# Optimization experiments

Measured on AMD Instinct MI355X. Metric: run time of the kernel, lower is better.

The kernel has to match this reference:

```python
import jax, jax.numpy as jnp
import numpy as np

N_NODES = 512
STATE_DIM = 16
MESSAGE_DIM = 32
HID_MSG = 64
HID_RO = 64
N_STEPS = 5


def setup_inputs() -> dict:
    key = jax.random.key(0)
    ks = jax.random.split(key, 16)
    s, m, hm, hr = STATE_DIM, MESSAGE_DIM, HID_MSG, HID_RO
    gru_in = s + m
    k_gru = 1.0 / np.sqrt(s)
    inp = {
        'J': jax.random.normal(ks[0], (N_NODES, N_NODES), jnp.float32),
        'b': jax.random.normal(ks[1], (N_NODES,), jnp.float32),
        # message MLP (torch init: weight ~ N(0, 0.1), bias = 0)
        'W1': 0.1 * jax.random.normal(ks[2], (hm, 2 * s + 3), jnp.float32),
        'b1': jnp.zeros((hm,), jnp.float32),
        'W2': 0.1 * jax.random.normal(ks[3], (hm, hm), jnp.float32),
        'b2': jnp.zeros((hm,), jnp.float32),
        'W3': 0.1 * jax.random.normal(ks[4], (m, hm), jnp.float32),
        'b3': jnp.zeros((m,), jnp.float32),
        # GRUCell params (torch default: U(-1/sqrt(hidden), 1/sqrt(hidden)))
        'W_ih': jax.random.uniform(ks[5], (3 * s, gru_in), jnp.float32, -k_gru, k_gru),
        'b_ih': jnp.zeros((3 * s,), jnp.float32),
        'W_hh': jax.random.uniform(ks[6], (3 * s, s), jnp.float32, -k_gru, k_gru),
        'b_hh': jnp.zeros((3 * s,), jnp.float32),
        # readout MLP
        'Wr1': 0.1 * jax.random.normal(ks[7], (hr, s), jnp.float32),
        'br1': jnp.zeros((hr,), jnp.float32),
        'Wr2': 0.1 * jax.random.normal(ks[8], (hr, hr), jnp.float32),
        'br2': jnp.zeros((hr,), jnp.float32),
        'Wr3': 0.1 * jax.random.normal(ks[9], (2, hr), jnp.float32),
        'br3': jnp.zeros((2,), jnp.float32),
    }
    return inp


def _gru_cell(x, h, W_ih, b_ih, W_hh, b_hh):
    s = h.shape[-1]
    gi = x @ W_ih.T + b_ih  # (n, 3s)
    gh = h @ W_hh.T + b_hh  # (n, 3s)
    ir, iz, in_ = gi[:, :s], gi[:, s:2 * s], gi[:, 2 * s:]
    hr, hz, hn = gh[:, :s], gh[:, s:2 * s], gh[:, 2 * s:]
    r = jax.nn.sigmoid(ir + hr)
    z = jax.nn.sigmoid(iz + hz)
    n = jnp.tanh(in_ + r * hn)
    return (1.0 - z) * n + z * h


def reference(J, b, W1, b1, W2, b2, W3, b3, W_ih, b_ih, W_hh, b_hh,
              Wr1, br1, Wr2, br2, Wr3, br3):
    n = J.shape[0]
    s = W_hh.shape[1]
    # Split first message-MLP layer by input blocks [h_i | h_j | J_ij | b_i | b_j]
    # so we never materialize the (n, n, 2s+3) feature tensor.
    W1_hi = W1[:, :s]            # (hm, s)
    W1_hj = W1[:, s:2 * s]       # (hm, s)
    w_J = W1[:, 2 * s]           # (hm,)
    w_bi = W1[:, 2 * s + 1]      # (hm,)
    w_bj = W1[:, 2 * s + 2]      # (hm,)
    # static per-pair part of layer-1 preactivation: (n, n, hm)
    static1 = (J[:, :, None] * w_J
               + b[:, None, None] * w_bi
               + b[None, :, None] * w_bj
               + b1)

    h0 = jnp.zeros((n, s), jnp.float32)

    def step(h, _):
        pre = (h @ W1_hi.T)[:, None, :] + (h @ W1_hj.T)[None, :, :] + static1
        x = jax.nn.relu(pre)                      # (n, n, hm)
        x = jax.nn.relu(x @ W2.T + b2)            # (n, n, hm)
        msg = x @ W3.T + b3                       # (n, n, m)
        m_j = msg.sum(axis=0)                     # sum over i -> (n, m)
        gru_in = jnp.concatenate([h, m_j], axis=1)
        h_new = _gru_cell(gru_in, h, W_ih, b_ih, W_hh, b_hh)
        return h_new, None

    h, _ = jax.lax.scan(step, h0, None, length=N_STEPS)

    y = jax.nn.relu(h @ Wr1.T + br1)
    y = jax.nn.relu(y @ Wr2.T + br2)
    y = jax.nn.sigmoid(y @ Wr3.T + br3)           # (n, 2)
    y = y / jnp.sum(y, axis=1, keepdims=True)
    return y
```

## Files before the change

### kernel.cpp

```cpp
#include <hip/hip_runtime.h>
#include <hip/hip_bf16.h>

#define NN 512
#define NSTEPS 5

typedef __attribute__((ext_vector_type(8))) short short8;
typedef __attribute__((ext_vector_type(4))) float floatx4;

static __device__ __forceinline__ unsigned short f2bf(float f) {
    union { float f; unsigned u; } x; x.f = f;
    unsigned r = x.u + 0x7fffu + ((x.u >> 16) & 1u);
    return (unsigned short)(r >> 16);
}

static __device__ __forceinline__ unsigned pk2bf(float a, float b) {
    __hip_bfloat162 h = __float22bfloat162_rn(make_float2(a, b));
    return *reinterpret_cast<unsigned*>(&h);
}

__global__ void init_kernel(const float* __restrict__ J, const float* __restrict__ b,
                            const float* __restrict__ W1, const float* __restrict__ b1,
                            const float* __restrict__ W2,
                            float* __restrict__ Jt, float* __restrict__ aG, float* __restrict__ cG,
                            float* __restrict__ h0, float* __restrict__ wJ,
                            float* __restrict__ wbi, float* __restrict__ wbj,
                            float* __restrict__ W1hiT, float* __restrict__ W1hjT,
                            unsigned short* __restrict__ W2bf)
{
    int bx = blockIdx.x, tid = threadIdx.x;
    if (bx < 64) {
        __shared__ float tile[64][65];
        int ti = bx >> 3, tj = bx & 7;
        for (int p = 0; p < 16; ++p) {
            int e = p*256 + tid; int r = e >> 6, c = e & 63;
            tile[r][c] = J[(ti*64 + r)*512 + tj*64 + c];
        }
        __syncthreads();
        for (int p = 0; p < 16; ++p) {
            int e = p*256 + tid; int r = e >> 6, c = e & 63;
            Jt[(tj*64 + r)*512 + ti*64 + c] = tile[c][r];
        }
    } else if (bx < 96) {
        int gid = (bx - 64)*256 + tid;
        for (int p = 0; p < 4; ++p) {
            int idx = p*8192 + gid;
            int i = idx >> 6, o = idx & 63;
            aG[idx] = b[i] * W1[o*35 + 33];
        }
    } else if (bx < 128) {
        int gid = (bx - 96)*256 + tid;
        for (int p = 0; p < 4; ++p) {
            int idx = p*8192 + gid;
            int i = idx >> 6, o = idx & 63;
            cG[idx] = b[i] * W1[o*35 + 34] + b1[o];
        }
    } else if (bx == 128) {
        for (int p = 0; p < 16; ++p) {
            int flat = p*256 + tid;
            int jj = flat & 7;
            int lane = (flat >> 3) & 63;
            int tk = flat >> 9;
            int nt = tk >> 1, ks = tk & 1;
            int n = nt*16 + (lane & 15);
            int k = ks*32 + (lane >> 4)*8 + jj;
            W2bf[flat] = f2bf(W2[n*64 + k]);
        }
        if (tid < 64) {
            wJ[tid]  = W1[tid*35 + 32];
            wbi[tid] = W1[tid*35 + 33];
            wbj[tid] = W1[tid*35 + 34];
            #pragma unroll
            for (int s = 0; s < 16; ++s) {
                W1hiT[tid*16 + s] = W1[tid*35 + s];
                W1hjT[tid*16 + s] = W1[tid*35 + 16 + s];
            }
        }
    } else {
        for (int p = 0; p < 32; ++p) h0[p*256 + tid] = 0.f;
    }
}

__global__ __launch_bounds__(256) void edge_kernel(
    const float* __restrict__ Jt,
    const float* __restrict__ aIn, const float* __restrict__ cIn, const float* __restrict__ hIn,
    float* __restrict__ aOut, float* __restrict__ cOut, float* __restrict__ hOut,
    const unsigned short* __restrict__ W2bf, const float* __restrict__ wJ,
    const float* __restrict__ b2, const float* __restrict__ W3, const float* __restrict__ b3,
    const float* __restrict__ W_ih, const float* __restrict__ b_ih,
    const float* __restrict__ W_hh, const float* __restrict__ b_hh,
    const float* __restrict__ W1hiT, const float* __restrict__ W1hjT,
    const float* __restrict__ wbi, const float* __restrict__ wbj,
    const float* __restrict__ bvec, const float* __restrict__ b1,
    const float* __restrict__ Wr1, const float* __restrict__ br1,
    const float* __restrict__ Wr2, const float* __restrict__ br2,
    const float* __restrict__ Wr3, const float* __restrict__ br3,
    float* __restrict__ out, int last)
{
    const int j = blockIdx.x;
    const int tid = threadIdx.x;
    const int l = tid & 63, w = tid >> 6;
    const int m = l & 15, q = l >> 4;

    __shared__ float smWave[4][64];
    __shared__ float smMacc[64];
    __shared__ float smGin[48];
    __shared__ float smGi[48], smGh[48];
    __shared__ float smH[16];
    __shared__ float smY[64];
    __shared__ float smR[2];

    const floatx4* c4 = (const floatx4*)cIn;
    const floatx4* w4 = (const floatx4*)wJ;
    floatx4 cva = c4[j*16 + q*2],     cvb = c4[j*16 + q*2 + 1];
    floatx4 cvc = c4[j*16 + 8 + q*2], cvd = c4[j*16 + 8 + q*2 + 1];
    floatx4 wva = w4[q*2], wvb = w4[q*2+1], wvc = w4[8+q*2], wvd = w4[8+q*2+1];

    short8 bfw[4][2];
    {
        const short8* wb = (const short8*)W2bf;
        #pragma unroll
        for (int nt = 0; nt < 4; ++nt)
            #pragma unroll
            for (int ks = 0; ks < 2; ++ks)
                bfw[nt][ks] = wb[(nt*2 + ks)*64 + l];
    }
    float b2n[4];
    #pragma unroll
    for (int nt = 0; nt < 4; ++nt) b2n[nt] = b2[nt*16 + m];

    floatx4 acc[4];
    #pragma unroll
    for (int nt = 0; nt < 4; ++nt) acc[nt] = (floatx4){0.f,0.f,0.f,0.f};

    const floatx4* a4 = (const floatx4*)aIn;

    for (int c8 = 0; c8 < 8; ++c8) {
        int i = w*128 + c8*16 + m;
        float Jij = Jt[j*512 + i];
        floatx4 av0 = a4[i*16 + q*2],     av1 = a4[i*16 + q*2 + 1];
        floatx4 av2 = a4[i*16 + 8 + q*2], av3 = a4[i*16 + 8 + q*2 + 1];
        floatx4 x0, x1, x2, x3;
        #pragma unroll
        for (int e = 0; e < 4; ++e) {
            x0[e] = fmaxf(fmaf(Jij, wva[e], av0[e]) + cva[e], 0.f);
            x1[e] = fmaxf(fmaf(Jij, wvb[e], av1[e]) + cvb[e], 0.f);
            x2[e] = fmaxf(fmaf(Jij, wvc[e], av2[e]) + cvc[e], 0.f);
            x3[e] = fmaxf(fmaf(Jij, wvd[e], av3[e]) + cvd[e], 0.f);
        }
        union { short8 s; unsigned u[4]; } fa0, fa1;
        fa0.u[0] = pk2bf(x0[0], x0[1]); fa0.u[1] = pk2bf(x0[2], x0[3]);
        fa0.u[2] = pk2bf(x1[0], x1[1]); fa0.u[3] = pk2bf(x1[2], x1[3]);
        fa1.u[0] = pk2bf(x2[0], x2[1]); fa1.u[1] = pk2bf(x2[2], x2[3]);
        fa1.u[2] = pk2bf(x3[0], x3[1]); fa1.u[3] = pk2bf(x3[2], x3[3]);
        #pragma unroll
        for (int nt = 0; nt < 4; ++nt) {
            floatx4 d = {0.f,0.f,0.f,0.f};
            d = __builtin_amdgcn_mfma_f32_16x16x32_bf16(fa0.s, bfw[nt][0], d, 0, 0, 0);
            d = __builtin_amdgcn_mfma_f32_16x16x32_bf16(fa1.s, bfw[nt][1], d, 0, 0, 0);
            #pragma unroll
            for (int r = 0; r < 4; ++r)
                acc[nt][r] += fmaxf(d[r] + b2n[nt], 0.f);
        }
    }

    #pragma unroll
    for (int nt = 0; nt < 4; ++nt) {
        float v = acc[nt][0] + acc[nt][1] + acc[nt][2] + acc[nt][3];
        v += __shfl_xor(v, 16);
        v += __shfl_xor(v, 32);
        if (l < 16) smWave[w][nt*16 + l] = v;
    }
    if (tid < 16) smGin[tid] = hIn[j*16 + tid];
    __syncthreads();
    if (tid < 64) smMacc[tid] = smWave[0][tid] + smWave[1][tid] + smWave[2][tid] + smWave[3][tid];
    __syncthreads();

    {
        int o = tid >> 3, p = tid & 7;
        const floatx4* W3v = (const floatx4*)W3;
        floatx4 wv0 = W3v[o*16 + p*2], wv1 = W3v[o*16 + p*2 + 1];
        float part = 0.f;
        #pragma unroll
        for (int e = 0; e < 4; ++e) {
            part = fmaf(wv0[e], smMacc[p*8 + e], part);
            part = fmaf(wv1[e], smMacc[p*8 + 4 + e], part);
        }
        part += __shfl_xor(part, 1);
        part += __shfl_xor(part, 2);
        part += __shfl_xor(part, 4);
        if (p == 0) smGin[16 + o] = part + 512.f * b3[o];
    }
    __syncthreads();

    if (tid < 192) {
        int o = tid >> 2, p = tid & 3;
        const floatx4* Wv = (const floatx4*)W_ih;
        floatx4 w0 = Wv[o*12 + p*3], w1 = Wv[o*12 + p*3 + 1], w2 = Wv[o*12 + p*3 + 2];
        int k0 = p*12;
        float part = 0.f;
        #pragma unroll
        for (int e = 0; e < 4; ++e) {
            part = fmaf(w0[e], smGin[k0 + e], part);
            part = fmaf(w1[e], smGin[k0 + 4 + e], part);
            part = fmaf(w2[e], smGin[k0 + 8 + e], part);
        }
        part += __shfl_xor(part, 1);
        part += __shfl_xor(part, 2);
        if (p == 0) smGi[o] = part + b_ih[o];
    } else if (tid < 240) {
        int o = tid - 192;
        const floatx4* Wv = (const floatx4*)W_hh;
        floatx4 w0 = Wv[o*4], w1 = Wv[o*4+1], w2 = Wv[o*4+2], w3 = Wv[o*4+3];
        float s = b_hh[o];
        #pragma unroll
        for (int e = 0; e < 4; ++e) {
            s = fmaf(w0[e], smGin[e],      s);
            s = fmaf(w1[e], smGin[4 + e],  s);
            s = fmaf(w2[e], smGin[8 + e],  s);
            s = fmaf(w3[e], smGin[12 + e], s);
        }
        smGh[o] = s;
    }
    __syncthreads();

    if (tid < 16) {
        float r = 1.f / (1.f + __expf(-(smGi[tid] + smGh[tid])));
        float z = 1.f / (1.f + __expf(-(smGi[16+tid] + smGh[16+tid])));
        float n = tanhf(smGi[32+tid] + r * smGh[32+tid]);
        float hn = (1.f - z)*n + z*smGin[tid];
        hOut[j*16 + tid] = hn;
        smH[tid] = hn;
    }
    __syncthreads();

    if (!last) {
        if (tid < 128) {
            int o = tid & 63, sel = tid >> 6;
            const floatx4* Wv = (const floatx4*)(sel ? W1hjT : W1hiT);
            floatx4 w0 = Wv[o*4], w1 = Wv[o*4+1], w2 = Wv[o*4+2], w3 = Wv[o*4+3];
            float s = 0.f;
            #pragma unroll
            for (int e = 0; e < 4; ++e) {
                s = fmaf(w0[e], smH[e],      s);
                s = fmaf(w1[e], smH[4 + e],  s);
                s = fmaf(w2[e], smH[8 + e],  s);
                s = fmaf(w3[e], smH[12 + e], s);
            }
            if (sel == 0) aOut[j*64 + o] = s + bvec[j]*wbi[o];
            else          cOut[j*64 + o] = s + bvec[j]*wbj[o] + b1[o];
        }
    } else {
        if (tid < 64) {
            const floatx4* Wv = (const floatx4*)Wr1;
            floatx4 w0 = Wv[tid*4], w1 = Wv[tid*4+1], w2 = Wv[tid*4+2], w3 = Wv[tid*4+3];
            float s = br1[tid];
            #pragma unroll
            for (int e = 0; e < 4; ++e) {
                s = fmaf(w0[e], smH[e],      s);
                s = fmaf(w1[e], smH[4 + e],  s);
                s = fmaf(w2[e], smH[8 + e],  s);
                s = fmaf(w3[e], smH[12 + e], s);
            }
            smY[tid] = fmaxf(s, 0.f);
        }
        __syncthreads();
        {
            int o = tid >> 2, p = tid & 3;
            const floatx4* Wv = (const floatx4*)Wr2;
            floatx4 w0 = Wv[o*16 + p*4],     w1 = Wv[o*16 + p*4 + 1];
            floatx4 w2 = Wv[o*16 + p*4 + 2], w3 = Wv[o*16 + p*4 + 3];
            int k0 = p*16;
            float part = 0.f;
            #pragma unroll
            for (int e = 0; e < 4; ++e) {
                part = fmaf(w0[e], smY[k0 + e],      part);
                part = fmaf(w1[e], smY[k0 + 4 + e],  part);
                part = fmaf(w2[e], smY[k0 + 8 + e],  part);
                part = fmaf(w3[e], smY[k0 + 12 + e], part);
            }
            part += __shfl_xor(part, 1);
            part += __shfl_xor(part, 2);
            __syncthreads();
            if (p == 0) smY[o] = fmaxf(part + br2[o], 0.f);
        }
        __syncthreads();
        if (tid < 128) {
            int ot = tid >> 6, p = tid & 63;
            float part = Wr3[ot*64 + p] * smY[p];
            part += __shfl_xor(part, 1);
            part += __shfl_xor(part, 2);
            part += __shfl_xor(part, 4);
            part += __shfl_xor(part, 8);
            part += __shfl_xor(part, 16);
            part += __shfl_xor(part, 32);
            if (p == 0) smR[ot] = part + br3[ot];
        }
        __syncthreads();
        if (tid == 0) {
            float e0 = 1.f/(1.f + __expf(-smR[0]));
            float e1 = 1.f/(1.f + __expf(-smR[1]));
            float t = e0 + e1;
            out[j*2]     = e0/t;
            out[j*2 + 1] = e1/t;
        }
    }
}

extern "C" void kernel_launch(void* const* d_in, const int* in_sizes, int n_in,
                              void* d_out, int out_size, void* d_ws, size_t ws_size,
                              hipStream_t stream)
{
    const float* J    = (const float*)d_in[0];
    const float* b    = (const float*)d_in[1];
    const float* W1   = (const float*)d_in[2];
    const float* b1   = (const float*)d_in[3];
    const float* W2   = (const float*)d_in[4];
    const float* b2   = (const float*)d_in[5];
    const float* W3   = (const float*)d_in[6];
    const float* b3   = (const float*)d_in[7];
    const float* W_ih = (const float*)d_in[8];
    const float* b_ih = (const float*)d_in[9];
    const float* W_hh = (const float*)d_in[10];
    const float* b_hh = (const float*)d_in[11];
    const float* Wr1  = (const float*)d_in[12];
    const float* br1  = (const float*)d_in[13];
    const float* Wr2  = (const float*)d_in[14];
    const float* br2  = (const float*)d_in[15];
    const float* Wr3  = (const float*)d_in[16];
    const float* br3  = (const float*)d_in[17];
    float* out = (float*)d_out;

    float* ws   = (float*)d_ws;
    float* Jt   = ws;
    float* aG0  = Jt + 262144;
    float* aG1  = aG0 + 32768;
    float* cG0  = aG1 + 32768;
    float* cG1  = cG0 + 32768;
    float* hA   = cG1 + 32768;
    float* hB   = hA + 8192;
    float* wJ   = hB + 8192;
    float* wbi  = wJ + 64;
    float* wbj  = wbi + 64;
    float* W1hiT = wbj + 64;
    float* W1hjT = W1hiT + 1024;
    unsigned short* W2bf = (unsigned short*)(W1hjT + 1024);

    hipLaunchKernelGGL(init_kernel, dim3(130), dim3(256), 0, stream,
                       J, b, W1, b1, W2, Jt, aG0, cG0, hA, wJ, wbi, wbj, W1hiT, W1hjT, W2bf);

    float* aIn = aG0; float* aOut = aG1;
    float* cIn = cG0; float* cOut = cG1;
    float* hI  = hA;  float* hO  = hB;
    for (int t = 0; t < NSTEPS; ++t) {
        hipLaunchKernelGGL(edge_kernel, dim3(512), dim3(256), 0, stream,
            Jt, aIn, cIn, hI, aOut, cOut, hO, W2bf, wJ, b2, W3, b3,
            W_ih, b_ih, W_hh, b_hh, W1hiT, W1hjT, wbi, wbj, b, b1,
            Wr1, br1, Wr2, br2, Wr3, br3, out, (t == NSTEPS-1) ? 1 : 0);
        float* tmp;
        tmp = aIn; aIn = aOut; aOut = tmp;
        tmp = cIn; cIn = cOut; cOut = tmp;
        tmp = hI;  hI  = hO;  hO  = tmp;
    }
}
```

Before: 159.0 us.

## Fuse init and all GRU steps into one persistent kernel with grid barriers

```diff
diff --git a/kernel.cpp b/kernel.cpp
--- a/kernel.cpp
+++ b/kernel.cpp
@@ -1,308 +1,345 @@
 #include <hip/hip_runtime.h>
 #include <hip/hip_bf16.h>
 
-#define NN 512
 #define NSTEPS 5
 
 typedef __attribute__((ext_vector_type(8))) short short8;
 typedef __attribute__((ext_vector_type(4))) float floatx4;
-
-static __device__ __forceinline__ unsigned short f2bf(float f) {
-    union { float f; unsigned u; } x; x.f = f;
-    unsigned r = x.u + 0x7fffu + ((x.u >> 16) & 1u);
-    return (unsigned short)(r >> 16);
-}
 
 static __device__ __forceinline__ unsigned pk2bf(float a, float b) {
     __hip_bfloat162 h = __float22bfloat162_rn(make_float2(a, b));
     return *reinterpret_cast<unsigned*>(&h);
 }
 
-__global__ void init_kernel(const float* __restrict__ J, const float* __restrict__ b,
-                            const float* __restrict__ W1, const float* __restrict__ b1,
-                            const float* __restrict__ W2,
-                            float* __restrict__ Jt, float* __restrict__ aG, float* __restrict__ cG,
-                            float* __restrict__ h0, float* __restrict__ wJ,
-                            float* __restrict__ wbi, float* __restrict__ wbj,
-                            float* __restrict__ W1hiT, float* __restrict__ W1hjT,
-                            unsigned short* __restrict__ W2bf)
+struct Params {
+    const float *J, *b, *W1, *b1, *W2, *b2, *W3, *b3;
+    const float *W_ih, *b_ih, *W_hh, *b_hh;
+    const float *Wr1, *br1, *Wr2, *br2, *Wr3, *br3;
+    float *out;
+    float *aA, *aB;
+    unsigned *bar;
+};
+
+static __device__ __forceinline__ void gbar(unsigned* bar, unsigned target) {
+    __threadfence();
+    __syncthreads();
+    if (threadIdx.x == 0) {
+        unsigned old = __hip_atomic_fetch_add(&bar[0], 1u, __ATOMIC_ACQ_REL,
+                                              __HIP_MEMORY_SCOPE_AGENT);
+        if (old == 255u) {
+            __hip_atomic_store(&bar[0], 0u, __ATOMIC_RELAXED, __HIP_MEMORY_SCOPE_AGENT);
+            __hip_atomic_fetch_add(&bar[1], 1u, __ATOMIC_RELEASE, __HIP_MEMORY_SCOPE_AGENT);
+        } else {
+            while (__hip_atomic_load(&bar[1], __ATOMIC_ACQUIRE,
+                                     __HIP_MEMORY_SCOPE_AGENT) < target) {
+                __builtin_amdgcn_s_sleep(1);
+            }
+        }
+    }
+    __syncthreads();
+    __threadfence();
+}
+
+__global__ __launch_bounds__(256, 2) void ggnn_fused(Params p)
 {
-    int bx = blockIdx.x, tid = threadIdx.x;
-    if (bx < 64) {
-        __shared__ float tile[64][65];
-        int ti = bx >> 3, tj = bx & 7;
-        for (int p = 0; p < 16; ++p) {
-            int e = p*256 + tid; int r = e >> 6, c = e & 63;
-            tile[r][c] = J[(ti*64 + r)*512 + tj*64 + c];
-        }
-        __syncthreads();
-        for (int p = 0; p < 16; ++p) {
-            int e = p*256 + tid; int r = e >> 6, c = e & 63;
-            Jt[(tj*64 + r)*512 + ti*64 + c] = tile[c][r];
-        }
-    } else if (bx < 96) {
-        int gid = (bx - 64)*256 + tid;
-        for (int p = 0; p < 4; ++p) {
-            int idx = p*8192 + gid;
-            int i = idx >> 6, o = idx & 63;
-            aG[idx] = b[i] * W1[o*35 + 33];
-        }
-    } else if (bx < 128) {
-        int gid = (bx - 96)*256 + tid;
-        for (int p = 0; p < 4; ++p) {
-            int idx = p*8192 + gid;
-            int i = idx >> 6, o = idx & 63;
-            cG[idx] = b[i] * W1[o*35 + 34] + b1[o];
-        }
-    } else if (bx == 128) {
-        for (int p = 0; p < 16; ++p) {
-            int flat = p*256 + tid;
-            int jj = flat & 7;
-            int lane = (flat >> 3) & 63;
-            int tk = flat >> 9;
-            int nt = tk >> 1, ks = tk & 1;
-            int n = nt*16 + (lane & 15);
-            int k = ks*32 + (lane >> 4)*8 + jj;
-            W2bf[flat] = f2bf(W2[n*64 + k]);
-        }
-        if (tid < 64) {
-            wJ[tid]  = W1[tid*35 + 32];
-            wbi[tid] = W1[tid*35 + 33];
-            wbj[tid] = W1[tid*35 + 34];
-            #pragma unroll
-            for (int s = 0; s < 16; ++s) {
-                W1hiT[tid*16 + s] = W1[tid*35 + s];
-                W1hjT[tid*16 + s] = W1[tid*35 + 16 + s];
-            }
-        }
-    } else {
-        for (int p = 0; p < 32; ++p) h0[p*256 + tid] = 0.f;
-    }
-}
-
-__global__ __launch_bounds__(256) void edge_kernel(
-    const float* __restrict__ Jt,
-    const float* __restrict__ aIn, const float* __restrict__ cIn, const float* __restrict__ hIn,
-    float* __restrict__ aOut, float* __restrict__ cOut, float* __restrict__ hOut,
-    const unsigned short* __restrict__ W2bf, const float* __restrict__ wJ,
-    const float* __restrict__ b2, const float* __restrict__ W3, const float* __restrict__ b3,
-    const float* __restrict__ W_ih, const float* __restrict__ b_ih,
-    const float* __restrict__ W_hh, const float* __restrict__ b_hh,
-    const float* __restrict__ W1hiT, const float* __restrict__ W1hjT,
-    const float* __restrict__ wbi, const float* __restrict__ wbj,
-    const float* __restrict__ bvec, const float* __restrict__ b1,
-    const float* __restrict__ Wr1, const float* __restrict__ br1,
-    const float* __restrict__ Wr2, const float* __restrict__ br2,
-    const float* __restrict__ Wr3, const float* __restrict__ br3,
-    float* __restrict__ out, int last)
-{
-    const int j = blockIdx.x;
     const int tid = threadIdx.x;
     const int l = tid & 63, w = tid >> 6;
     const int m = l & 15, q = l >> 4;
-
-    __shared__ float smWave[4][64];
-    __shared__ float smMacc[64];
-    __shared__ float smGin[48];
-    __shared__ float smGi[48], smGh[48];
-    __shared__ float smH[16];
-    __shared__ float smY[64];
-    __shared__ float smR[2];
-
-    const floatx4* c4 = (const floatx4*)cIn;
-    const floatx4* w4 = (const floatx4*)wJ;
-    floatx4 cva = c4[j*16 + q*2],     cvb = c4[j*16 + q*2 + 1];
-    floatx4 cvc = c4[j*16 + 8 + q*2], cvd = c4[j*16 + 8 + q*2 + 1];
-    floatx4 wva = w4[q*2], wvb = w4[q*2+1], wvc = w4[8+q*2], wvd = w4[8+q*2+1];
+    const int j0 = blockIdx.x, j1 = blockIdx.x + 256;
+
+    __shared__ __align__(16) float smJ[2][512];
+    __shared__ __align__(16) float smW1hi[64][16];
+    __shared__ __align__(16) float smW1hj[64][16];
+    __shared__ __align__(16) float smwJ[64], smwbi[64], smwbj[64], smb1[64];
+    __shared__ __align__(16) float smC[2][64];
+    __shared__ __align__(16) float smH[2][16];
+    __shared__ __align__(16) float smWave[2][4][64];
+    __shared__ __align__(16) float smMacc[2][64];
+    __shared__ __align__(16) float smGin[2][48];
+    __shared__ __align__(16) float smGi[2][48];
+    __shared__ __align__(16) float smGh[2][48];
+    __shared__ __align__(16) float smY[2][64];
+    __shared__ __align__(16) float smY2[2][64];
+    __shared__ float smR[2][2];
+
+    #pragma unroll
+    for (int r = 0; r < 2; ++r) {
+        int i = r * 256 + tid;
+        smJ[0][i] = p.J[i * 512 + j0];
+        smJ[1][i] = p.J[i * 512 + j1];
+    }
+    if (tid < 64) {
+        int o = tid;
+        #pragma unroll
+        for (int s = 0; s < 16; ++s) {
+            smW1hi[o][s] = p.W1[o * 35 + s];
+            smW1hj[o][s] = p.W1[o * 35 + 16 + s];
+        }
+        smwJ[o]  = p.W1[o * 35 + 32];
+        smwbi[o] = p.W1[o * 35 + 33];
+        smwbj[o] = p.W1[o * 35 + 34];
+        smb1[o]  = p.b1[o];
+    }
 
     short8 bfw[4][2];
-    {
-        const short8* wb = (const short8*)W2bf;
-        #pragma unroll
-        for (int nt = 0; nt < 4; ++nt)
-            #pragma unroll
-            for (int ks = 0; ks < 2; ++ks)
-                bfw[nt][ks] = wb[(nt*2 + ks)*64 + l];
-    }
     float b2n[4];
-    #pragma unroll
-    for (int nt = 0; nt < 4; ++nt) b2n[nt] = b2[nt*16 + m];
-
-    floatx4 acc[4];
-    #pragma unroll
-    for (int nt = 0; nt < 4; ++nt) acc[nt] = (floatx4){0.f,0.f,0.f,0.f};
-
-    const floatx4* a4 = (const floatx4*)aIn;
-
-    for (int c8 = 0; c8 < 8; ++c8) {
-        int i = w*128 + c8*16 + m;
-        float Jij = Jt[j*512 + i];
-        floatx4 av0 = a4[i*16 + q*2],     av1 = a4[i*16 + q*2 + 1];
-        floatx4 av2 = a4[i*16 + 8 + q*2], av3 = a4[i*16 + 8 + q*2 + 1];
-        floatx4 x0, x1, x2, x3;
-        #pragma unroll
-        for (int e = 0; e < 4; ++e) {
-            x0[e] = fmaxf(fmaf(Jij, wva[e], av0[e]) + cva[e], 0.f);
-            x1[e] = fmaxf(fmaf(Jij, wvb[e], av1[e]) + cvb[e], 0.f);
-            x2[e] = fmaxf(fmaf(Jij, wvc[e], av2[e]) + cvc[e], 0.f);
-            x3[e] = fmaxf(fmaf(Jij, wvd[e], av3[e]) + cvd[e], 0.f);
-        }
-        union { short8 s; unsigned u[4]; } fa0, fa1;
-        fa0.u[0] = pk2bf(x0[0], x0[1]); fa0.u[1] = pk2bf(x0[2], x0[3]);
-        fa0.u[2] = pk2bf(x1[0], x1[1]); fa0.u[3] = pk2bf(x1[2], x1[3]);
-        fa1.u[0] = pk2bf(x2[0], x2[1]); fa1.u[1] = pk2bf(x2[2], x2[3]);
-        fa1.u[2] = pk2bf(x3[0], x3[1]); fa1.u[3] = pk2bf(x3[2], x3[3]);
+    {
+        const floatx4* W2v = (const floatx4*)p.W2;
         #pragma unroll
         for (int nt = 0; nt < 4; ++nt) {
-            floatx4 d = {0.f,0.f,0.f,0.f};
-            d = __builtin_amdgcn_mfma_f32_16x16x32_bf16(fa0.s, bfw[nt][0], d, 0, 0, 0);
-            d = __builtin_amdgcn_mfma_f32_16x16x32_bf16(fa1.s, bfw[nt][1], d, 0, 0, 0);
-            #pragma unroll
-            for (int r = 0; r < 4; ++r)
-                acc[nt][r] += fmaxf(d[r] + b2n[nt], 0.f);
-        }
-    }
-
-    #pragma unroll
-    for (int nt = 0; nt < 4; ++nt) {
-        float v = acc[nt][0] + acc[nt][1] + acc[nt][2] + acc[nt][3];
-        v += __shfl_xor(v, 16);
-        v += __shfl_xor(v, 32);
-        if (l < 16) smWave[w][nt*16 + l] = v;
-    }
-    if (tid < 16) smGin[tid] = hIn[j*16 + tid];
-    __syncthreads();
-    if (tid < 64) smMacc[tid] = smWave[0][tid] + smWave[1][tid] + smWave[2][tid] + smWave[3][tid];
-    __syncthreads();
-
-    {
-        int o = tid >> 3, p = tid & 7;
-        const floatx4* W3v = (const floatx4*)W3;
-        floatx4 wv0 = W3v[o*16 + p*2], wv1 = W3v[o*16 + p*2 + 1];
+            int n = nt * 16 + m;
+            #pragma unroll
+            for (int ks = 0; ks < 2; ++ks) {
+                int kb = ks * 32 + q * 8;
+                floatx4 f0 = W2v[n * 16 + (kb >> 2)];
+                floatx4 f1 = W2v[n * 16 + (kb >> 2) + 1];
+                union { short8 s; unsigned u[4]; } t;
+                t.u[0] = pk2bf(f0[0], f0[1]); t.u[1] = pk2bf(f0[2], f0[3]);
+                t.u[2] = pk2bf(f1[0], f1[1]); t.u[3] = pk2bf(f1[2], f1[3]);
+                bfw[nt][ks] = t.s;
+            }
+            b2n[nt] = p.b2[nt * 16 + m];
+        }
+    }
+    __syncthreads();
+
+    float bj[2] = { p.b[j0], p.b[j1] };
+
+    floatx4 wva, wvb, wvc, wvd;
+    {
+        const floatx4* wv4 = (const floatx4*)smwJ;
+        wva = wv4[q * 2];     wvb = wv4[q * 2 + 1];
+        wvc = wv4[8 + q * 2]; wvd = wv4[8 + q * 2 + 1];
+    }
+
+    if (tid < 128) {
+        int col = tid >> 6, o = tid & 63;
+        int jc = col ? j1 : j0;
+        p.aA[jc * 64 + o] = bj[col] * smwbi[o];
+        smC[col][o] = bj[col] * smwbj[o] + smb1[o];
+    }
+    if (tid < 32) smH[tid >> 4][tid & 15] = 0.f;
+
+    gbar(p.bar, 1);
+
+    const float* aIn = p.aA;
+    float* aOut = p.aB;
+
+    for (int t = 0; t < NSTEPS; ++t) {
+        const floatx4* c40 = (const floatx4*)&smC[0][0];
+        const floatx4* c41 = (const floatx4*)&smC[1][0];
+        floatx4 cva0 = c40[q*2], cvb0 = c40[q*2+1], cvc0 = c40[8+q*2], cvd0 = c40[8+q*2+1];
+        floatx4 cva1 = c41[q*2], cvb1 = c41[q*2+1], cvc1 = c41[8+q*2], cvd1 = c41[8+q*2+1];
+
+        floatx4 acc[2][4];
+        #pragma unroll
+        for (int col = 0; col < 2; ++col)
+            #pragma unroll
+            for (int nt = 0; nt < 4; ++nt) acc[col][nt] = (floatx4){0.f,0.f,0.f,0.f};
+
+        const floatx4* a4 = (const floatx4*)aIn;
+
+        for (int c8 = 0; c8 < 8; ++c8) {
+            int i = w * 128 + c8 * 16 + m;
+            float J0 = smJ[0][i], J1 = smJ[1][i];
+            floatx4 av0 = a4[i*16 + q*2],     av1 = a4[i*16 + q*2 + 1];
+            floatx4 av2 = a4[i*16 + 8 + q*2], av3 = a4[i*16 + 8 + q*2 + 1];
+
+            floatx4 x0, x1, x2, x3;
+            union { short8 s; unsigned u[4]; } fa0, fa1, fb0, fb1;
+            #pragma unroll
+            for (int e = 0; e < 4; ++e) {
+                x0[e] = fmaxf(fmaf(J0, wva[e], av0[e]) + cva0[e], 0.f);
+                x1[e] = fmaxf(fmaf(J0, wvb[e], av1[e]) + cvb0[e], 0.f);
+                x2[e] = fmaxf(fmaf(J0, wvc[e], av2[e]) + cvc0[e], 0.f);
+                x3[e] = fmaxf(fmaf(J0, wvd[e], av3[e]) + cvd0[e], 0.f);
+            }
+            fa0.u[0] = pk2bf(x0[0], x0[1]); fa0.u[1] = pk2bf(x0[2], x0[3]);
+            fa0.u[2] = pk2bf(x1[0], x1[1]); fa0.u[3] = pk2bf(x1[2], x1[3]);
+            fa1.u[0] = pk2bf(x2[0], x2[1]); fa1.u[1] = pk2bf(x2[2], x2[3]);
+            fa1.u[2] = pk2bf(x3[0], x3[1]); fa1.u[3] = pk2bf(x3[2], x3[3]);
+            #pragma unroll
+            for (int e = 0; e < 4; ++e) {
+                x0[e] = fmaxf(fmaf(J1, wva[e], av0[e]) + cva1[e], 0.f);
+                x1[e] = fmaxf(fmaf(J1, wvb[e], av1[e]) + cvb1[e], 0.f);
+                x2[e] = fmaxf(fmaf(J1, wvc[e], av2[e]) + cvc1[e], 0.f);
+                x3[e] = fmaxf(fmaf(J1, wvd[e], av3[e]) + cvd1[e], 0.f);
+            }
+            fb0.u[0] = pk2bf(x0[0], x0[1]); fb0.u[1] = pk2bf(x0[2], x0[3]);
+            fb0.u[2] = pk2bf(x1[0], x1[1]); fb0.u[3] = pk2bf(x1[2], x1[3]);
+            fb1.u[0] = pk2bf(x2[0], x2[1]); fb1.u[1] = pk2bf(x2[2], x2[3]);
+            fb1.u[2] = pk2bf(x3[0], x3[1]); fb1.u[3] = pk2bf(x3[2], x3[3]);
+
+            #pragma unroll
+            for (int nt = 0; nt < 4; ++nt) {
+                floatx4 d = {0.f,0.f,0.f,0.f};
+                d = __builtin_amdgcn_mfma_f32_16x16x32_bf16(fa0.s, bfw[nt][0], d, 0, 0, 0);
+                d = __builtin_amdgcn_mfma_f32_16x16x32_bf16(fa1.s, bfw[nt][1], d, 0, 0, 0);
+                floatx4 d2 = {0.f,0.f,0.f,0.f};
+                d2 = __builtin_amdgcn_mfma_f32_16x16x32_bf16(fb0.s, bfw[nt][0], d2, 0, 0, 0);
+                d2 = __builtin_amdgcn_mfma_f32_16x16x32_bf16(fb1.s, bfw[nt][1], d2, 0, 0, 0);
+                #pragma unroll
+                for (int r = 0; r < 4; ++r) {
+                    acc[0][nt][r] += fmaxf(d[r]  + b2n[nt], 0.f);
+                    acc[1][nt][r] += fmaxf(d2[r] + b2n[nt], 0.f);
+                }
+            }
+        }
+
+        #pragma unroll
+        for (int col = 0; col < 2; ++col)
+            #pragma unroll
+            for (int nt = 0; nt < 4; ++nt) {
+                float v = acc[col][nt][0] + acc[col][nt][1] + acc[col][nt][2] + acc[col][nt][3];
+                v += __shfl_xor(v, 16);
+                v += __shfl_xor(v, 32);
+                if (l < 16) smWave[col][w][nt*16 + l] = v;
+            }
+        if (tid < 32) smGin[tid >> 4][tid & 15] = smH[tid >> 4][tid & 15];
+        __syncthreads();
+        if (tid < 128) {
+            int col = tid >> 6, o = tid & 63;
+            smMacc[col][o] = smWave[col][0][o] + smWave[col][1][o]
+                           + smWave[col][2][o] + smWave[col][3][o];
+        }
+        __syncthreads();
+
+        {
+            int col = tid >> 7, t2 = tid & 127;
+            int o = t2 >> 2, pp = t2 & 3;
+            const floatx4* W3v = (const floatx4*)p.W3;
+            floatx4 w0 = W3v[o*16 + pp*4],     w1 = W3v[o*16 + pp*4 + 1];
+            floatx4 w2 = W3v[o*16 + pp*4 + 2], w3 = W3v[o*16 + pp*4 + 3];
+            float part = 0.f;
+            #pragma unroll
+            for (int e = 0; e < 4; ++e) {
+                part = fmaf(w0[e], smMacc[col][pp*16 + e],      part);
+                part = fmaf(w1[e], smMacc[col][pp*16 + 4 + e],  part);
+                part = fmaf(w2[e], smMacc[col][pp*16 + 8 + e],  part);
+                part = fmaf(w3[e], smMacc[col][pp*16 + 12 + e], part);
+            }
+            part += __shfl_xor(part, 1);
+            part += __shfl_xor(part, 2);
+            if (pp == 0) smGin[col][16 + o] = part + 512.f * p.b3[o];
+        }
+        __syncthreads();
+
+        {
+            int col = tid >> 7, t2 = tid & 127;
+            if (t2 < 48) {
+                const floatx4* Wv = (const floatx4*)p.W_ih;
+                const floatx4* g4 = (const floatx4*)&smGin[col][0];
+                float s = p.b_ih[t2];
+                #pragma unroll
+                for (int e = 0; e < 12; ++e) {
+                    floatx4 we = Wv[t2*12 + e], ge = g4[e];
+                    s = fmaf(we[0], ge[0], s); s = fmaf(we[1], ge[1], s);
+                    s = fmaf(we[2], ge[2], s); s = fmaf(we[3], ge[3], s);
+                }
+                smGi[col][t2] = s;
+            } else if (t2 >= 64 && t2 < 112) {
+                int o = t2 - 64;
+                const floatx4* Wv = (const floatx4*)p.W_hh;
+                const floatx4* h4 = (const floatx4*)&smGin[col][0];
+                float s = p.b_hh[o];
+                #pragma unroll
+                for (int e = 0; e < 4; ++e) {
+                    floatx4 we = Wv[o*4 + e], he = h4[e];
+                    s = fmaf(we[0], he[0], s); s = fmaf(we[1], he[1], s);
+                    s = fmaf(we[2], he[2], s); s = fmaf(we[3], he[3], s);
+                }
+                smGh[col][o] = s;
+            }
+        }
+        __syncthreads();
+
+        if (tid < 32) {
+            int col = tid >> 4, o = tid & 15;
+            float r = 1.f / (1.f + __expf(-(smGi[col][o] + smGh[col][o])));
+            float z = 1.f / (1.f + __expf(-(smGi[col][16+o] + smGh[col][16+o])));
+            float n = tanhf(smGi[col][32+o] + r * smGh[col][32+o]);
+            smH[col][o] = (1.f - z) * n + z * smGin[col][o];
+        }
+        __syncthreads();
+
+        if (t < NSTEPS - 1) {
+            {
+                int col = tid >> 7, t2 = tid & 127, o = t2 & 63, sel = t2 >> 6;
+                const floatx4* Wv = (const floatx4*)(sel ? &smW1hj[0][0] : &smW1hi[0][0]);
+                const floatx4* h4 = (const floatx4*)&smH[col][0];
+                floatx4 w0 = Wv[o*4], w1 = Wv[o*4+1], w2 = Wv[o*4+2], w3 = Wv[o*4+3];
+                float s = 0.f;
+                #pragma unroll
+                for (int e = 0; e < 4; ++e) {
+                    s = fmaf(w0[e], h4[0][e], s);
+                    s = fmaf(w1[e], h4[1][e], s);
+                    s = fmaf(w2[e], h4[2][e], s);
+                    s = fmaf(w3[e], h4[3][e], s);
+                }
+                int jc = col ? j1 : j0;
+                if (sel == 0) aOut[jc*64 + o] = s + bj[col] * smwbi[o];
+                else          smC[col][o]     = s + bj[col] * smwbj[o] + smb1[o];
+            }
+            gbar(p.bar, (unsigned)(t + 2));
+            const float* tmp = aIn; aIn = aOut; aOut = (float*)tmp;
+        }
+    }
+
+    {
+        int col = tid >> 7, t2 = tid & 127;
+        if (t2 < 64) {
+            const floatx4* Wv = (const floatx4*)p.Wr1;
+            const floatx4* h4 = (const floatx4*)&smH[col][0];
+            floatx4 w0 = Wv[t2*4], w1 = Wv[t2*4+1], w2 = Wv[t2*4+2], w3 = Wv[t2*4+3];
+            float s = p.br1[t2];
+            #pragma unroll
+            for (int e = 0; e < 4; ++e) {
+                s = fmaf(w0[e], h4[0][e], s);
+                s = fmaf(w1[e], h4[1][e], s);
+                s = fmaf(w2[e], h4[2][e], s);
+                s = fmaf(w3[e], h4[3][e], s);
+            }
+            smY[col][t2] = fmaxf(s, 0.f);
+        }
+    }
+    __syncthreads();
+    {
+        int col = tid >> 7, t2 = tid & 127;
+        int o = t2 >> 1, pp = t2 & 1;
+        const floatx4* Wv = (const floatx4*)p.Wr2;
+        const floatx4* y4 = (const floatx4*)&smY[col][0];
         float part = 0.f;
         #pragma unroll
-        for (int e = 0; e < 4; ++e) {
-            part = fmaf(wv0[e], smMacc[p*8 + e], part);
-            part = fmaf(wv1[e], smMacc[p*8 + 4 + e], part);
-        }
+        for (int e = 0; e < 8; ++e) {
+            floatx4 we = Wv[o*16 + pp*8 + e], ye = y4[pp*8 + e];
+            part = fmaf(we[0], ye[0], part); part = fmaf(we[1], ye[1], part);
+            part = fmaf(we[2], ye[2], part); part = fmaf(we[3], ye[3], part);
+        }
+        part += __shfl_xor(part, 1);
+        if (pp == 0) smY2[col][o] = fmaxf(part + p.br2[o], 0.f);
+    }
+    __syncthreads();
+    {
+        int col = tid >> 7, t2 = tid & 127;
+        int ot = t2 >> 6, pp = t2 & 63;
+        float part = p.Wr3[ot*64 + pp] * smY2[col][pp];
         part += __shfl_xor(part, 1);
         part += __shfl_xor(part, 2);
         part += __shfl_xor(part, 4);
-        if (p == 0) smGin[16 + o] = part + 512.f * b3[o];
-    }
-    __syncthreads();
-
-    if (tid < 192) {
-        int o = tid >> 2, p = tid & 3;
-        const floatx4* Wv = (const floatx4*)W_ih;
-        floatx4 w0 = Wv[o*12 + p*3], w1 = Wv[o*12 + p*3 + 1], w2 = Wv[o*12 + p*3 + 2];
-        int k0 = p*12;
-        float part = 0.f;
-        #pragma unroll
-        for (int e = 0; e < 4; ++e) {
-            part = fmaf(w0[e], smGin[k0 + e], part);
-            part = fmaf(w1[e], smGin[k0 + 4 + e], part);
-            part = fmaf(w2[e], smGin[k0 + 8 + e], part);
-        }
-        part += __shfl_xor(part, 1);
-        part += __shfl_xor(part, 2);
-        if (p == 0) smGi[o] = part + b_ih[o];
-    } else if (tid < 240) {
-        int o = tid - 192;
-        const floatx4* Wv = (const floatx4*)W_hh;
-        floatx4 w0 = Wv[o*4], w1 = Wv[o*4+1], w2 = Wv[o*4+2], w3 = Wv[o*4+3];
-        float s = b_hh[o];
-        #pragma unroll
-        for (int e = 0; e < 4; ++e) {
-            s = fmaf(w0[e], smGin[e],      s);
-            s = fmaf(w1[e], smGin[4 + e],  s);
-            s = fmaf(w2[e], smGin[8 + e],  s);
-            s = fmaf(w3[e], smGin[12 + e], s);
-        }
-        smGh[o] = s;
-    }
-    __syncthreads();
-
-    if (tid < 16) {
-        float r = 1.f / (1.f + __expf(-(smGi[tid] + smGh[tid])));
-        float z = 1.f / (1.f + __expf(-(smGi[16+tid] + smGh[16+tid])));
-        float n = tanhf(smGi[32+tid] + r * smGh[32+tid]);
-        float hn = (1.f - z)*n + z*smGin[tid];
-        hOut[j*16 + tid] = hn;
-        smH[tid] = hn;
-    }
-    __syncthreads();
-
-    if (!last) {
-        if (tid < 128) {
-            int o = tid & 63, sel = tid >> 6;
-            const floatx4* Wv = (const floatx4*)(sel ? W1hjT : W1hiT);
-            floatx4 w0 = Wv[o*4], w1 = Wv[o*4+1], w2 = Wv[o*4+2], w3 = Wv[o*4+3];
-            float s = 0.f;
-            #pragma unroll
-            for (int e = 0; e < 4; ++e) {
-                s = fmaf(w0[e], smH[e],      s);
-                s = fmaf(w1[e], smH[4 + e],  s);
-                s = fmaf(w2[e], smH[8 + e],  s);
-                s = fmaf(w3[e], smH[12 + e], s);
-            }
-            if (sel == 0) aOut[j*64 + o] = s + bvec[j]*wbi[o];
-            else          cOut[j*64 + o] = s + bvec[j]*wbj[o] + b1[o];
-        }
-    } else {
-        if (tid < 64) {
-            const floatx4* Wv = (const floatx4*)Wr1;
-            floatx4 w0 = Wv[tid*4], w1 = Wv[tid*4+1], w2 = Wv[tid*4+2], w3 = Wv[tid*4+3];
-            float s = br1[tid];
-            #pragma unroll
-            for (int e = 0; e < 4; ++e) {
-                s = fmaf(w0[e], smH[e],      s);
-                s = fmaf(w1[e], smH[4 + e],  s);
-                s = fmaf(w2[e], smH[8 + e],  s);
-                s = fmaf(w3[e], smH[12 + e], s);
-            }
-            smY[tid] = fmaxf(s, 0.f);
-        }
-        __syncthreads();
-        {
-            int o = tid >> 2, p = tid & 3;
-            const floatx4* Wv = (const floatx4*)Wr2;
-            floatx4 w0 = Wv[o*16 + p*4],     w1 = Wv[o*16 + p*4 + 1];
-            floatx4 w2 = Wv[o*16 + p*4 + 2], w3 = Wv[o*16 + p*4 + 3];
-            int k0 = p*16;
-            float part = 0.f;
-            #pragma unroll
-            for (int e = 0; e < 4; ++e) {
-                part = fmaf(w0[e], smY[k0 + e],      part);
-                part = fmaf(w1[e], smY[k0 + 4 + e],  part);
-                part = fmaf(w2[e], smY[k0 + 8 + e],  part);
-                part = fmaf(w3[e], smY[k0 + 12 + e], part);
-            }
-            part += __shfl_xor(part, 1);
-            part += __shfl_xor(part, 2);
-            __syncthreads();
-            if (p == 0) smY[o] = fmaxf(part + br2[o], 0.f);
-        }
-        __syncthreads();
-        if (tid < 128) {
-            int ot = tid >> 6, p = tid & 63;
-            float part = Wr3[ot*64 + p] * smY[p];
-            part += __shfl_xor(part, 1);
-            part += __shfl_xor(part, 2);
-            part += __shfl_xor(part, 4);
-            part += __shfl_xor(part, 8);
-            part += __shfl_xor(part, 16);
-            part += __shfl_xor(part, 32);
-            if (p == 0) smR[ot] = part + br3[ot];
-        }
-        __syncthreads();
-        if (tid == 0) {
-            float e0 = 1.f/(1.f + __expf(-smR[0]));
-            float e1 = 1.f/(1.f + __expf(-smR[1]));
-            float t = e0 + e1;
-            out[j*2]     = e0/t;
-            out[j*2 + 1] = e1/t;
-        }
+        part += __shfl_xor(part, 8);
+        part += __shfl_xor(part, 16);
+        part += __shfl_xor(part, 32);
+        if (pp == 0) smR[col][ot] = part + p.br3[ot];
+    }
+    __syncthreads();
+    if (tid < 2) {
+        int col = tid;
+        int jc = col ? j1 : j0;
+        float e0 = 1.f / (1.f + __expf(-smR[col][0]));
+        float e1 = 1.f / (1.f + __expf(-smR[col][1]));
+        float tsum = e0 + e1;
+        p.out[jc*2]     = e0 / tsum;
+        p.out[jc*2 + 1] = e1 / tsum;
     }
 }
 
@@ -310,55 +347,32 @@
                               void* d_out, int out_size, void* d_ws, size_t ws_size,
                               hipStream_t stream)
 {
-    const float* J    = (const float*)d_in[0];
-    const float* b    = (const float*)d_in[1];
-    const float* W1   = (const float*)d_in[2];
-    const float* b1   = (const float*)d_in[3];
-    const float* W2   = (const float*)d_in[4];
-    const float* b2   = (const float*)d_in[5];
-    const float* W3   = (const float*)d_in[6];
-    const float* b3   = (const float*)d_in[7];
-    const float* W_ih = (const float*)d_in[8];
-    const float* b_ih = (const float*)d_in[9];
-    const float* W_hh = (const float*)d_in[10];
-    const float* b_hh = (const float*)d_in[11];
-    const float* Wr1  = (const float*)d_in[12];
-    const float* br1  = (const float*)d_in[13];
-    const float* Wr2  = (const float*)d_in[14];
-    const float* br2  = (const float*)d_in[15];
-    const float* Wr3  = (const float*)d_in[16];
-    const float* br3  = (const float*)d_in[17];
-    float* out = (float*)d_out;
-
-    float* ws   = (float*)d_ws;
-    float* Jt   = ws;
-    float* aG0  = Jt + 262144;
-    float* aG1  = aG0 + 32768;
-    float* cG0  = aG1 + 32768;
-    float* cG1  = cG0 + 32768;
-    float* hA   = cG1 + 32768;
-    float* hB   = hA + 8192;
-    float* wJ   = hB + 8192;
-    float* wbi  = wJ + 64;
-    float* wbj  = wbi + 64;
-    float* W1hiT = wbj + 64;
-    float* W1hjT = W1hiT + 1024;
-    unsigned short* W2bf = (unsigned short*)(W1hjT + 1024);
-
-    hipLaunchKernelGGL(init_kernel, dim3(130), dim3(256), 0, stream,
-                       J, b, W1, b1, W2, Jt, aG0, cG0, hA, wJ, wbi, wbj, W1hiT, W1hjT, W2bf);
-
-    float* aIn = aG0; float* aOut = aG1;
-    float* cIn = cG0; float* cOut = cG1;
-    float* hI  = hA;  float* hO  = hB;
-    for (int t = 0; t < NSTEPS; ++t) {
-        hipLaunchKernelGGL(edge_kernel, dim3(512), dim3(256), 0, stream,
-            Jt, aIn, cIn, hI, aOut, cOut, hO, W2bf, wJ, b2, W3, b3,
-            W_ih, b_ih, W_hh, b_hh, W1hiT, W1hjT, wbi, wbj, b, b1,
-            Wr1, br1, Wr2, br2, Wr3, br3, out, (t == NSTEPS-1) ? 1 : 0);
-        float* tmp;
-        tmp = aIn; aIn = aOut; aOut = tmp;
-        tmp = cIn; cIn = cOut; cOut = tmp;
-        tmp = hI;  hI  = hO;  hO  = tmp;
-    }
+    Params par;
+    par.J    = (const float*)d_in[0];
+    par.b    = (const float*)d_in[1];
+    par.W1   = (const float*)d_in[2];
+    par.b1   = (const float*)d_in[3];
+    par.W2   = (const float*)d_in[4];
+    par.b2   = (const float*)d_in[5];
+    par.W3   = (const float*)d_in[6];
+    par.b3   = (const float*)d_in[7];
+    par.W_ih = (const float*)d_in[8];
+    par.b_ih = (const float*)d_in[9];
+    par.W_hh = (const float*)d_in[10];
+    par.b_hh = (const float*)d_in[11];
+    par.Wr1  = (const float*)d_in[12];
+    par.br1  = (const float*)d_in[13];
+    par.Wr2  = (const float*)d_in[14];
+    par.br2  = (const float*)d_in[15];
+    par.Wr3  = (const float*)d_in[16];
+    par.br3  = (const float*)d_in[17];
+    par.out  = (float*)d_out;
+
+    float* ws = (float*)d_ws;
+    par.aA  = ws;
+    par.aB  = ws + 512 * 64;
+    par.bar = (unsigned*)(ws + 2 * 512 * 64);
+
+    hipMemsetAsync(par.bar, 0, 64, stream);
+    hipLaunchKernelGGL(ggnn_fused, dim3(256), dim3(256), 0, stream, par);
 }
```

After: 362.1 us. +127.8%, slower.
